# Kernel optimization log

Measured on AMD Instinct MI355X. Metric: run time of the kernel, lower is better.

Reference implementation:

```python
import jax, jax.numpy as jnp
import numpy as np

B, S, HID = 4, 1024, 2048
H, KV, D = 16, 4, 128  # query heads, kv heads, head_dim
ROPE_THETA = 1e6


def setup_inputs() -> dict:
    key = jax.random.key(0)
    ks = jax.random.split(key, 5)
    x = jax.random.normal(ks[0], (B, S, HID), dtype=jnp.float32)
    wq = jax.random.normal(ks[1], (HID, H * D), dtype=jnp.float32) / np.sqrt(HID)
    wk = jax.random.normal(ks[2], (HID, KV * D), dtype=jnp.float32) / np.sqrt(HID)
    wv = jax.random.normal(ks[3], (HID, KV * D), dtype=jnp.float32) / np.sqrt(HID)
    wo = jax.random.normal(ks[4], (H * D, HID), dtype=jnp.float32) / np.sqrt(H * D)
    # RoPE tables: freqs duplicated to head_dim (HF convention matching rotate_half)
    inv_freq = 1.0 / (ROPE_THETA ** (jnp.arange(0, D, 2, dtype=jnp.float32) / D))
    ang = jnp.arange(S, dtype=jnp.float32)[:, None] * inv_freq[None, :]  # [S, D/2]
    emb = jnp.concatenate([ang, ang], axis=-1)  # [S, D]
    return {"x": x, "cos": jnp.cos(emb), "sin": jnp.sin(emb),
            "wq": wq, "wk": wk, "wv": wv, "wo": wo}


def _rotate_half(t):
    half = t.shape[-1] // 2
    return jnp.concatenate([-t[..., half:], t[..., :half]], axis=-1)


def reference(x, cos, sin, wq, wk, wv, wo):
    b, s, _ = x.shape
    q = (x @ wq).reshape(b, s, H, D)
    k = (x @ wk).reshape(b, s, KV, D)
    v = (x @ wv).reshape(b, s, KV, D)
    # RoPE: cos/sin [S,D] broadcast over heads (unsqueeze_dim=1 -> [S,1,D])
    c = cos[:, None, :]
    sn = sin[:, None, :]
    q = q * c + _rotate_half(q) * sn
    k = k * c + _rotate_half(k) * sn
    # repeat_kv: each kv head repeated n_repeat times consecutively
    rep = H // KV
    k = jnp.repeat(k, rep, axis=2)  # [B,S,H,D]
    v = jnp.repeat(v, rep, axis=2)
    # [B,H,S,D]
    q = q.transpose(0, 2, 1, 3)
    k = k.transpose(0, 2, 1, 3)
    v = v.transpose(0, 2, 1, 3)
    scores = jnp.einsum("bhqd,bhkd->bhqk", q, k) / jnp.sqrt(jnp.float32(D))
    causal = jnp.tril(jnp.ones((s, s), dtype=bool))
    scores = jnp.where(causal, scores, -jnp.inf)
    probs = jax.nn.softmax(scores.astype(jnp.float32), axis=-1).astype(q.dtype)
    out = jnp.einsum("bhqk,bhkd->bhqd", probs, v)
    out = out.transpose(0, 2, 1, 3).reshape(b, s, H * D)
    return out @ wo
```

## Files before the change

kernel.cpp:

```cpp
#include <hip/hip_runtime.h>

typedef __attribute__((ext_vector_type(8))) __bf16 bf16x8;
typedef __attribute__((ext_vector_type(4))) __bf16 bf16x4;
typedef __attribute__((ext_vector_type(4))) float f32x4;

#define DEV static __device__ __forceinline__

DEV void gload_lds16(const void* g, void* l) {
  __builtin_amdgcn_global_load_lds((const __attribute__((address_space(1))) void*)g,
                                   (__attribute__((address_space(3))) void*)l, 16, 0, 0);
}

DEV void lgkm0_sb() {
  asm volatile("s_waitcnt lgkmcnt(0)" ::: "memory");
  __builtin_amdgcn_sched_barrier(0);
}

__global__ void cvt_kernel(const float* __restrict__ src, __bf16* __restrict__ dst, int n) {
  int i = (blockIdx.x * 256 + threadIdx.x) * 8;
  if (i >= n) return;
  float4 a = *(const float4*)(src + i);
  float4 b = *(const float4*)(src + i + 4);
  bf16x8 o;
  o[0] = (__bf16)a.x; o[1] = (__bf16)a.y; o[2] = (__bf16)a.z; o[3] = (__bf16)a.w;
  o[4] = (__bf16)b.x; o[5] = (__bf16)b.y; o[6] = (__bf16)b.z; o[7] = (__bf16)b.w;
  *(bf16x8*)(dst + i) = o;
}

__global__ void tcvt_kernel(const float* __restrict__ src, __bf16* __restrict__ dst, int K, int N) {
  __shared__ float tile[32][33];
  int k0 = blockIdx.y * 32, n0 = blockIdx.x * 32;
  int tx = threadIdx.x & 31, ty = threadIdx.x >> 5;
  #pragma unroll
  for (int i = 0; i < 32; i += 8)
    tile[ty + i][tx] = src[(size_t)(k0 + ty + i) * N + n0 + tx];
  __syncthreads();
  #pragma unroll
  for (int i = 0; i < 32; i += 8)
    dst[(size_t)(n0 + ty + i) * K + k0 + tx] = (__bf16)tile[tx][ty + i];
}

__global__ void vt_kernel(const __bf16* __restrict__ QKV, __bf16* __restrict__ VT) {
  __shared__ __bf16 t[32][33];
  int sx = blockIdx.x;
  int dx = blockIdx.y;
  int bk = blockIdx.z;
  int b = bk >> 2, kvh = bk & 3;
  int tx = threadIdx.x & 31, ty = threadIdx.x >> 5;
  #pragma unroll
  for (int i = 0; i < 32; i += 8)
    t[ty + i][tx] = QKV[(size_t)(b * 1024 + sx * 32 + ty + i) * 3072 + 2560 + kvh * 128 + dx * 32 + tx];
  __syncthreads();
  #pragma unroll
  for (int i = 0; i < 32; i += 8)
    VT[((size_t)bk * 128 + dx * 32 + ty + i) * 1024 + sx * 32 + tx] = t[tx][ty + i];
}

template <int BM, typename OutT>
__global__ __launch_bounds__(512, 2) void gemm8p(const __bf16* __restrict__ A,
                                                 const __bf16* __restrict__ Bt,
                                                 OutT* __restrict__ C,
                                                 int M, int N, int K) {
  constexpr int ABYTES = BM * 64 * 2;
  constexpr int BBYTES = 256 * 64 * 2;
  constexpr int MH = BM / 64;
  __shared__ alignas(1024) char smem[2 * (ABYTES + BBYTES)];

  const int tid = threadIdx.x;
  const int l = tid & 63, w = tid >> 6;
  const int wr = w >> 2, wc = w & 3;
  const int g = l >> 4, ln = l & 15;

  const int nbx = gridDim.x;
  const int nwg = nbx * gridDim.y;
  int lin = blockIdx.y * nbx + blockIdx.x;
  lin = (lin & 7) * (nwg >> 3) + (lin >> 3);
  const int brow = (lin / nbx) * BM, bcol = (lin % nbx) * 256;

  const __bf16* Ag = A + (size_t)brow * K;
  const __bf16* Bg = Bt + (size_t)bcol * K;
  const int NT = K / 64;

  auto Abuf = [&](int buf) -> char* { return smem + buf * ABYTES; };
  auto Bbuf = [&](int buf) -> char* { return smem + 2 * ABYTES + buf * BBYTES; };

  f32x4 acc[2 * MH][4] = {};

  auto chunk = [&](const __bf16* gb, char* lb, int ktc, int sub) {
    int r16 = l >> 2;
    int colb = ((l & 3) * 16) ^ (((l >> 5) & 1) << 5);
    int row = (sub >> 1) * 16 + r16;
    gload_lds16(gb + (size_t)row * K + ktc * 64 + (sub & 1) * 32 + (colb >> 1),
                lb + sub * 1024 + l * 16);
  };
  auto stA0 = [&](int ktc, int buf) {
    if constexpr (BM == 256) {
      #pragma unroll
      for (int i = 0; i < 2; ++i) { int idx = i * 8 + w; chunk(Ag, Abuf(buf), ktc, (idx >> 3) * 16 + (idx & 7)); }
    } else {
      chunk(Ag, Abuf(buf), ktc, (w >> 2) * 8 + (w & 3));
    }
  };
  auto stA1 = [&](int ktc, int buf) {
    if constexpr (BM == 256) {
      #pragma unroll
      for (int i = 0; i < 2; ++i) { int idx = i * 8 + w; chunk(Ag, Abuf(buf), ktc, 8 + (idx >> 3) * 16 + (idx & 7)); }
    } else {
      chunk(Ag, Abuf(buf), ktc, 4 + (w >> 2) * 8 + (w & 3));
    }
  };
  auto stB0 = [&](int ktc, int buf) {
    #pragma unroll
    for (int i = 0; i < 2; ++i) { int idx = i * 8 + w; chunk(Bg, Bbuf(buf), ktc, (idx >> 2) * 8 + (idx & 3)); }
  };
  auto stB1 = [&](int ktc, int buf) {
    #pragma unroll
    for (int i = 0; i < 2; ++i) { int idx = i * 8 + w; chunk(Bg, Bbuf(buf), ktc, 4 + (idx >> 2) * 8 + (idx & 3)); }
  };

  auto ldA = [&](int buf, int m, int kk) -> bf16x8 {
    int sub = (wr * (BM / 32) + m) * 2 + kk;
    return *(const bf16x8*)(Abuf(buf) + sub * 1024 + ln * 64 + ((g * 16) ^ (((ln >> 3) & 1) << 5)));
  };
  auto ldB = [&](int buf, int n, int kk) -> bf16x8 {
    int sub = (wc * 4 + n) * 2 + kk;
    return *(const bf16x8*)(Bbuf(buf) + sub * 1024 + ln * 64 + ((g * 16) ^ (((ln >> 3) & 1) << 5)));
  };

  auto vmw = [&](int which) {
    if constexpr (BM == 256) {
      if (which == 0) asm volatile("s_waitcnt vmcnt(10)" ::: "memory");
      else if (which == 1) asm volatile("s_waitcnt vmcnt(12)" ::: "memory");
      else asm volatile("s_waitcnt vmcnt(12)" ::: "memory");
    } else {
      if (which == 0) asm volatile("s_waitcnt vmcnt(7)" ::: "memory");
      else if (which == 1) asm volatile("s_waitcnt vmcnt(9)" ::: "memory");
      else asm volatile("s_waitcnt vmcnt(9)" ::: "memory");
    }
    __builtin_amdgcn_sched_barrier(0);
  };
  auto bar = [&]() {
    __builtin_amdgcn_sched_barrier(0);
    __builtin_amdgcn_s_barrier();
    __builtin_amdgcn_sched_barrier(0);
  };

  stA0(0, 0); stB0(0, 0); stB1(0, 0); stA1(0, 0);
  stA0(1, 1); stB0(1, 1); stB1(1, 1); stA1(1, 1);
  vmw(2);
  bar();

  bf16x8 af[MH][2], bf[4][2];

  for (int kt = 0; kt < NT; ++kt) {
    const int buf = kt & 1;
    const int ktc = (kt + 2) & 31;

    #pragma unroll
    for (int m = 0; m < MH; ++m) { af[m][0] = ldA(buf, m, 0); af[m][1] = ldA(buf, m, 1); }
    #pragma unroll
    for (int n = 0; n < 2; ++n) { bf[n][0] = ldB(buf, n, 0); bf[n][1] = ldB(buf, n, 1); }
    bar();
    lgkm0_sb();
    __builtin_amdgcn_s_setprio(1);
    #pragma unroll
    for (int m = 0; m < MH; ++m)
      #pragma unroll
      for (int n = 0; n < 2; ++n)
        #pragma unroll
        for (int kk = 0; kk < 2; ++kk)
          acc[m][n] = __builtin_amdgcn_mfma_f32_16x16x32_bf16(af[m][kk], bf[n][kk], acc[m][n], 0, 0, 0);
    __builtin_amdgcn_s_setprio(0);
    vmw(0);
    bar();

    #pragma unroll
    for (int n = 2; n < 4; ++n) { bf[n][0] = ldB(buf, n, 0); bf[n][1] = ldB(buf, n, 1); }
    stA0(ktc, buf); stB0(ktc, buf);
    bar();
    lgkm0_sb();
    __builtin_amdgcn_s_setprio(1);
    #pragma unroll
    for (int m = 0; m < MH; ++m)
      #pragma unroll
      for (int n = 2; n < 4; ++n)
        #pragma unroll
        for (int kk = 0; kk < 2; ++kk)
          acc[m][n] = __builtin_amdgcn_mfma_f32_16x16x32_bf16(af[m][kk], bf[n][kk], acc[m][n], 0, 0, 0);
    __builtin_amdgcn_s_setprio(0);
    vmw(1);
    bar();

    #pragma unroll
    for (int m = 0; m < MH; ++m) { af[m][0] = ldA(buf, MH + m, 0); af[m][1] = ldA(buf, MH + m, 1); }
    stB1(ktc, buf);
    bar();
    lgkm0_sb();
    __builtin_amdgcn_s_setprio(1);
    #pragma unroll
    for (int m = 0; m < MH; ++m)
      #pragma unroll
      for (int n = 0; n < 2; ++n)
        #pragma unroll
        for (int kk = 0; kk < 2; ++kk)
          acc[MH + m][n] = __builtin_amdgcn_mfma_f32_16x16x32_bf16(af[m][kk], bf[n][kk], acc[MH + m][n], 0, 0, 0);
    __builtin_amdgcn_s_setprio(0);
    bar();

    stA1(ktc, buf);
    bar();
    lgkm0_sb();
    __builtin_amdgcn_s_setprio(1);
    #pragma unroll
    for (int m = 0; m < MH; ++m)
      #pragma unroll
      for (int n = 2; n < 4; ++n)
        #pragma unroll
        for (int kk = 0; kk < 2; ++kk)
          acc[MH + m][n] = __builtin_amdgcn_mfma_f32_16x16x32_bf16(af[m][kk], bf[n][kk], acc[MH + m][n], 0, 0, 0);
    __builtin_amdgcn_s_setprio(0);
    vmw(2);
    bar();
  }

  #pragma unroll
  for (int mi = 0; mi < 2 * MH; ++mi)
    #pragma unroll
    for (int n = 0; n < 4; ++n)
      #pragma unroll
      for (int j = 0; j < 4; ++j) {
        size_t r = brow + wr * (BM / 2) + mi * 16 + g * 4 + j;
        size_t c = bcol + wc * 64 + n * 16 + ln;
        C[r * N + c] = (OutT)acc[mi][n][j];
      }
}

__global__ void rope_kernel(__bf16* __restrict__ QKV, const float* __restrict__ cosb,
                            const float* __restrict__ sinb) {
  int gid = blockIdx.x * 256 + threadIdx.x;
  int p = gid & 15;
  int ht = gid >> 4;
  int hc = ht % 20;
  int tok = ht / 20;
  int s = tok & 1023;
  int colb = hc < 16 ? hc * 128 : 2048 + (hc - 16) * 128;
  __bf16* base = QKV + (size_t)tok * 3072 + colb;
  int d0 = p * 4;
  const float* cr = cosb + s * 128;
  const float* sr = sinb + s * 128;
  float x0[4], x1[4];
  #pragma unroll
  for (int j = 0; j < 4; ++j) {
    x0[j] = (float)base[d0 + j];
    x1[j] = (float)base[d0 + 64 + j];
  }
  #pragma unroll
  for (int j = 0; j < 4; ++j) {
    float n0 = x0[j] * cr[d0 + j] - x1[j] * sr[d0 + j];
    float n1 = x1[j] * cr[d0 + 64 + j] + x0[j] * sr[d0 + 64 + j];
    base[d0 + j] = (__bf16)n0;
    base[d0 + 64 + j] = (__bf16)n1;
  }
}

__global__ __launch_bounds__(256, 2) void attn_kernel(const __bf16* __restrict__ QKV,
                                                      const __bf16* __restrict__ VT,
                                                      __bf16* __restrict__ AO) {
  __shared__ __bf16 Kl[2][64 * 128];
  __shared__ __bf16 Vt[128 * 64];
  __shared__ __bf16 Pl[4][16 * 72];

  const int tid = threadIdx.x, l = tid & 63, w = tid >> 6;
  const int h = blockIdx.y, b = blockIdx.z;
  const int kvh = h >> 2;
  const int g = l >> 4, ln = l & 15;
  const __bf16* VTg = VT + (size_t)(b * 4 + kvh) * 128 * 1024;
  const float scsc = 0.08838834764831845f;

  auto stageK = [&](int buf, int kt) {
    const __bf16* Kg = QKV + (size_t)(b * 1024 + kt * 64) * 3072 + 2048 + kvh * 128;
    #pragma unroll
    for (int i = 0; i < 4; ++i) {
      int r = i * 16 + (tid >> 4);
      int c = tid & 15;
      int csw = c ^ (r & 7);
      gload_lds16(Kg + (size_t)r * 3072 + csw * 8, (char*)&Kl[buf][0] + i * 4096 + tid * 16);
    }
  };
  auto stageV = [&](int kt) {
    #pragma unroll
    for (int i = 0; i < 4; ++i) {
      int ci = i * 256 + tid;
      int row = ci >> 3;
      int c = ci & 7;
      int csw = c ^ (row & 7);
      gload_lds16(VTg + (size_t)row * 1024 + kt * 64 + csw * 8, (char*)Vt + (size_t)ci * 16);
    }
  };

  #pragma unroll 1
  for (int pass = 0; pass < 2; ++pass) {
    const int qt = pass ? 15 - (int)blockIdx.x : (int)blockIdx.x;
    const size_t tokQ = (size_t)b * 1024 + qt * 64;

    bf16x8 qf[4];
    {
      const __bf16* qp = QKV + (tokQ + w * 16 + ln) * 3072 + h * 128;
      #pragma unroll
      for (int ks = 0; ks < 4; ++ks) qf[ks] = *(const bf16x8*)(qp + ks * 32 + g * 8);
    }

    float mrow = -1e30f, lrow = 0.f;
    f32x4 acco[8] = {};

    stageK(0, 0);
    int cur = 0;

    for (int kt = 0; kt <= qt; ++kt) {
      __syncthreads();

      stageV(kt);
      if (kt < qt) stageK(cur ^ 1, kt + 1);

      f32x4 accs[4] = {};
      __builtin_amdgcn_s_setprio(1);
      #pragma unroll
      for (int cb = 0; cb < 4; ++cb) {
        int row = cb * 16 + ln;
        #pragma unroll
        for (int ks = 0; ks < 4; ++ks) {
          bf16x8 kb = *(const bf16x8*)((const char*)&Kl[cur][0] + row * 256 +
                                       (((ks * 4 + g) ^ (row & 7)) * 16));
          accs[cb] = __builtin_amdgcn_mfma_f32_16x16x32_bf16(kb, qf[ks], accs[cb], 0, 0, 0);
        }
      }
      __builtin_amdgcn_s_setprio(0);

      const bool diag = (kt == qt);
      #pragma unroll
      for (int cb = 0; cb < 4; ++cb)
        #pragma unroll
        for (int j = 0; j < 4; ++j) {
          float s = accs[cb][j] * scsc;
          if (diag && (cb * 16 + g * 4 + j > w * 16 + ln)) s = -1e30f;
          accs[cb][j] = s;
        }

      float mt = accs[0][0];
      #pragma unroll
      for (int cb = 0; cb < 4; ++cb)
        #pragma unroll
        for (int j = 0; j < 4; ++j) mt = fmaxf(mt, accs[cb][j]);
      mt = fmaxf(mt, __shfl_xor(mt, 16, 64));
      mt = fmaxf(mt, __shfl_xor(mt, 32, 64));
      float mnew = fmaxf(mrow, mt);
      float corr = __expf(mrow - mnew);
      mrow = mnew;
      float rs = 0.f;
      #pragma unroll
      for (int cb = 0; cb < 4; ++cb)
        #pragma unroll
        for (int j = 0; j < 4; ++j) {
          float p = __expf(accs[cb][j] - mnew);
          accs[cb][j] = p;
          rs += p;
        }
      rs += __shfl_xor(rs, 16, 64);
      rs += __shfl_xor(rs, 32, 64);
      lrow = lrow * corr + rs;
      #pragma unroll
      for (int n = 0; n < 8; ++n)
        #pragma unroll
        for (int j = 0; j < 4; ++j) acco[n][j] *= corr;

      #pragma unroll
      for (int cb = 0; cb < 4; ++cb) {
        bf16x4 pw;
        #pragma unroll
        for (int j = 0; j < 4; ++j) pw[j] = (__bf16)accs[cb][j];
        *(bf16x4*)(&Pl[w][ln * 72 + cb * 16 + g * 4]) = pw;
      }

      __syncthreads();

      __builtin_amdgcn_s_setprio(1);
      #pragma unroll
      for (int sc = 0; sc < 2; ++sc) {
        bf16x8 pa = *(const bf16x8*)(&Pl[w][ln * 72 + sc * 32 + g * 8]);
        #pragma unroll
        for (int n = 0; n < 8; ++n) {
          int row = n * 16 + ln;
          bf16x8 vb = *(const bf16x8*)((const char*)Vt + row * 128 +
                                       (((sc * 4 + g) ^ (row & 7)) * 16));
          acco[n] = __builtin_amdgcn_mfma_f32_16x16x32_bf16(vb, pa, acco[n], 0, 0, 0);
        }
      }
      __builtin_amdgcn_s_setprio(0);
      cur ^= 1;
    }

    float rl = 1.f / lrow;
    size_t r = tokQ + w * 16 + ln;
    #pragma unroll
    for (int n = 0; n < 8; ++n) {
      bf16x4 ov;
      #pragma unroll
      for (int j = 0; j < 4; ++j) ov[j] = (__bf16)(acco[n][j] * rl);
      *(bf16x4*)(&AO[r * 2048 + h * 128 + n * 16 + g * 4]) = ov;
    }
  }
}

extern "C" void kernel_launch(void* const* d_in, const int* in_sizes, int n_in,
                              void* d_out, int out_size, void* d_ws, size_t ws_size,
                              hipStream_t stream) {
  const float* x    = (const float*)d_in[0];
  const float* cosb = (const float*)d_in[1];
  const float* sinb = (const float*)d_in[2];
  const float* wq   = (const float*)d_in[3];
  const float* wk   = (const float*)d_in[4];
  const float* wv   = (const float*)d_in[5];
  const float* wo   = (const float*)d_in[6];
  float* out = (float*)d_out;

  char* ws = (char*)d_ws;
  const size_t OFF_XB    = 0;
  const size_t OFF_WQKVT = OFF_XB + 16777216;
  const size_t OFF_WOT   = OFF_WQKVT + 12582912;
  const size_t OFF_QKV   = OFF_WOT + 8388608;
  const size_t OFF_AO    = OFF_QKV + 25165824;
  const size_t OFF_VT    = OFF_XB;

  __bf16* Xb    = (__bf16*)(ws + OFF_XB);
  __bf16* WqkvT = (__bf16*)(ws + OFF_WQKVT);
  __bf16* WoT   = (__bf16*)(ws + OFF_WOT);
  __bf16* QKVb  = (__bf16*)(ws + OFF_QKV);
  __bf16* AOb   = (__bf16*)(ws + OFF_AO);
  __bf16* VTb   = (__bf16*)(ws + OFF_VT);

  cvt_kernel<<<4096 * 2048 / 8 / 256, 256, 0, stream>>>(x, Xb, 4096 * 2048);
  tcvt_kernel<<<dim3(64, 64), 256, 0, stream>>>(wq, WqkvT, 2048, 2048);
  tcvt_kernel<<<dim3(16, 64), 256, 0, stream>>>(wk, WqkvT + (size_t)2048 * 2048, 2048, 512);
  tcvt_kernel<<<dim3(16, 64), 256, 0, stream>>>(wv, WqkvT + (size_t)2560 * 2048, 2048, 512);
  tcvt_kernel<<<dim3(64, 64), 256, 0, stream>>>(wo, WoT, 2048, 2048);
  gemm8p<256, __bf16><<<dim3(12, 16), 512, 0, stream>>>(Xb, WqkvT, QKVb, 4096, 3072, 2048);
  vt_kernel<<<dim3(32, 4, 16), 256, 0, stream>>>(QKVb, VTb);
  rope_kernel<<<4096 * 20 * 16 / 256, 256, 0, stream>>>(QKVb, cosb, sinb);
  attn_kernel<<<dim3(8, 16, 4), 256, 0, stream>>>(QKVb, VTb, AOb);
  gemm8p<128, float><<<dim3(8, 32), 512, 0, stream>>>(AOb, WoT, out, 4096, 2048, 2048);
}
```

Measured before the change: 175.3 us.

## Add dedicated 256x192-tile QKV GEMM so the grid fills all CUs

Adds a specialized QKV projection GEMM that uses 256x192 output tiles instead of 256x256, raising the grid from 192 to 256 workgroups so all 256 CUs on the MI355X get work. It reorganizes the staged global-to-LDS loads, the MFMA sub-phases and the vmcnt wait counts for the 3-wide N fragment per wave. The cost is some loss of data reuse per tile and hand-tuned wait counts, and the kernel hardcodes the K-tile wraparound ((kt+2)&31), so it assumes K=2048.

Result: no change. 172.3 us (-1.7%).

```diff
diff --git a/kernel.cpp b/kernel.cpp
--- a/kernel.cpp
+++ b/kernel.cpp
@@ -232,6 +232,166 @@
         size_t r = brow + wr * (BM / 2) + mi * 16 + g * 4 + j;
         size_t c = bcol + wc * 64 + n * 16 + ln;
         C[r * N + c] = (OutT)acc[mi][n][j];
+      }
+}
+
+__global__ __launch_bounds__(512, 2) void gemm8p_qkv(const __bf16* __restrict__ A,
+                                                     const __bf16* __restrict__ Bt,
+                                                     __bf16* __restrict__ C,
+                                                     int M, int N, int K) {
+  constexpr int ABYTES = 256 * 64 * 2;
+  constexpr int BBYTES = 192 * 64 * 2;
+  __shared__ alignas(1024) char smem[2 * (ABYTES + BBYTES)];
+
+  const int tid = threadIdx.x;
+  const int l = tid & 63, w = tid >> 6;
+  const int wr = w >> 2, wc = w & 3;
+  const int g = l >> 4, ln = l & 15;
+
+  const int nbx = gridDim.x;
+  const int nwg = nbx * gridDim.y;
+  int lin = blockIdx.y * nbx + blockIdx.x;
+  lin = (lin & 7) * (nwg >> 3) + (lin >> 3);
+  const int brow = (lin / nbx) * 256, bcol = (lin % nbx) * 192;
+
+  const __bf16* Ag = A + (size_t)brow * K;
+  const __bf16* Bg = Bt + (size_t)bcol * K;
+  const int NT = K / 64;
+
+  auto Abuf = [&](int buf) -> char* { return smem + buf * ABYTES; };
+  auto Bbuf = [&](int buf) -> char* { return smem + 2 * ABYTES + buf * BBYTES; };
+
+  f32x4 acc[8][3] = {};
+
+  auto chunk = [&](const __bf16* gb, char* lb, int ktc, int sub) {
+    int r16 = l >> 2;
+    int colb = ((l & 3) * 16) ^ (((l >> 5) & 1) << 5);
+    int row = (sub >> 1) * 16 + r16;
+    gload_lds16(gb + (size_t)row * K + ktc * 64 + (sub & 1) * 32 + (colb >> 1),
+                lb + sub * 1024 + l * 16);
+  };
+  auto stA0 = [&](int ktc, int buf) {
+    #pragma unroll
+    for (int i = 0; i < 2; ++i) { int idx = i * 8 + w; chunk(Ag, Abuf(buf), ktc, (idx >> 3) * 16 + (idx & 7)); }
+  };
+  auto stA1 = [&](int ktc, int buf) {
+    #pragma unroll
+    for (int i = 0; i < 2; ++i) { int idx = i * 8 + w; chunk(Ag, Abuf(buf), ktc, 8 + (idx >> 3) * 16 + (idx & 7)); }
+  };
+  auto stBg0 = [&](int ktc, int buf) {
+    #pragma unroll
+    for (int i = 0; i < 2; ++i) {
+      int t = i * 8 + w;
+      int sub = ((t >> 2) * 3 + ((t >> 1) & 1)) * 2 + (t & 1);
+      chunk(Bg, Bbuf(buf), ktc, sub);
+    }
+  };
+  auto stBg1 = [&](int ktc, int buf) {
+    int sub = ((w >> 1) * 3 + 2) * 2 + (w & 1);
+    chunk(Bg, Bbuf(buf), ktc, sub);
+  };
+
+  auto ldA = [&](int buf, int m, int kk) -> bf16x8 {
+    int sub = (wr * 8 + m) * 2 + kk;
+    return *(const bf16x8*)(Abuf(buf) + sub * 1024 + ln * 64 + ((g * 16) ^ (((ln >> 3) & 1) << 5)));
+  };
+  auto ldB = [&](int buf, int nf, int kk) -> bf16x8 {
+    int sub = (wc * 3 + nf) * 2 + kk;
+    return *(const bf16x8*)(Bbuf(buf) + sub * 1024 + ln * 64 + ((g * 16) ^ (((ln >> 3) & 1) << 5)));
+  };
+
+  auto bar = [&]() {
+    __builtin_amdgcn_sched_barrier(0);
+    __builtin_amdgcn_s_barrier();
+    __builtin_amdgcn_sched_barrier(0);
+  };
+
+  stA0(0, 0); stBg0(0, 0); stBg1(0, 0); stA1(0, 0);
+  stA0(1, 1); stBg0(1, 1); stBg1(1, 1); stA1(1, 1);
+  asm volatile("s_waitcnt vmcnt(10)" ::: "memory");
+  __builtin_amdgcn_sched_barrier(0);
+  bar();
+
+  bf16x8 af[4][2], bfv[3][2];
+
+  for (int kt = 0; kt < NT; ++kt) {
+    const int buf = kt & 1;
+    const int ktc = (kt + 2) & 31;
+
+    #pragma unroll
+    for (int m = 0; m < 4; ++m) { af[m][0] = ldA(buf, m, 0); af[m][1] = ldA(buf, m, 1); }
+    #pragma unroll
+    for (int nf = 0; nf < 2; ++nf) { bfv[nf][0] = ldB(buf, nf, 0); bfv[nf][1] = ldB(buf, nf, 1); }
+    bar();
+    lgkm0_sb();
+    __builtin_amdgcn_s_setprio(1);
+    #pragma unroll
+    for (int m = 0; m < 4; ++m)
+      #pragma unroll
+      for (int nf = 0; nf < 2; ++nf)
+        #pragma unroll
+        for (int kk = 0; kk < 2; ++kk)
+          acc[m][nf] = __builtin_amdgcn_mfma_f32_16x16x32_bf16(af[m][kk], bfv[nf][kk], acc[m][nf], 0, 0, 0);
+    __builtin_amdgcn_s_setprio(0);
+    asm volatile("s_waitcnt vmcnt(9)" ::: "memory");
+    __builtin_amdgcn_sched_barrier(0);
+    bar();
+
+    bfv[2][0] = ldB(buf, 2, 0); bfv[2][1] = ldB(buf, 2, 1);
+    stA0(ktc, buf); stBg0(ktc, buf);
+    bar();
+    lgkm0_sb();
+    __builtin_amdgcn_s_setprio(1);
+    #pragma unroll
+    for (int m = 0; m < 4; ++m)
+      #pragma unroll
+      for (int kk = 0; kk < 2; ++kk)
+        acc[m][2] = __builtin_amdgcn_mfma_f32_16x16x32_bf16(af[m][kk], bfv[2][kk], acc[m][2], 0, 0, 0);
+    __builtin_amdgcn_s_setprio(0);
+    asm volatile("s_waitcnt vmcnt(11)" ::: "memory");
+    __builtin_amdgcn_sched_barrier(0);
+    bar();
+
+    #pragma unroll
+    for (int m = 0; m < 4; ++m) { af[m][0] = ldA(buf, 4 + m, 0); af[m][1] = ldA(buf, 4 + m, 1); }
+    stBg1(ktc, buf);
+    bar();
+    lgkm0_sb();
+    __builtin_amdgcn_s_setprio(1);
+    #pragma unroll
+    for (int m = 0; m < 4; ++m)
+      #pragma unroll
+      for (int nf = 0; nf < 2; ++nf)
+        #pragma unroll
+        for (int kk = 0; kk < 2; ++kk)
+          acc[4 + m][nf] = __builtin_amdgcn_mfma_f32_16x16x32_bf16(af[m][kk], bfv[nf][kk], acc[4 + m][nf], 0, 0, 0);
+    __builtin_amdgcn_s_setprio(0);
+    bar();
+
+    stA1(ktc, buf);
+    bar();
+    lgkm0_sb();
+    __builtin_amdgcn_s_setprio(1);
+    #pragma unroll
+    for (int m = 0; m < 4; ++m)
+      #pragma unroll
+      for (int kk = 0; kk < 2; ++kk)
+        acc[4 + m][2] = __builtin_amdgcn_mfma_f32_16x16x32_bf16(af[m][kk], bfv[2][kk], acc[4 + m][2], 0, 0, 0);
+    __builtin_amdgcn_s_setprio(0);
+    asm volatile("s_waitcnt vmcnt(10)" ::: "memory");
+    __builtin_amdgcn_sched_barrier(0);
+    bar();
+  }
+
+  #pragma unroll
+  for (int mi = 0; mi < 8; ++mi)
+    #pragma unroll
+    for (int nf = 0; nf < 3; ++nf)
+      #pragma unroll
+      for (int j = 0; j < 4; ++j) {
+        size_t r = brow + wr * 128 + mi * 16 + g * 4 + j;
+        size_t c = bcol + wc * 48 + nf * 16 + ln;
+        C[r * N + c] = (__bf16)acc[mi][nf][j];
       }
 }
 
@@ -443,7 +603,7 @@
   tcvt_kernel<<<dim3(16, 64), 256, 0, stream>>>(wk, WqkvT + (size_t)2048 * 2048, 2048, 512);
   tcvt_kernel<<<dim3(16, 64), 256, 0, stream>>>(wv, WqkvT + (size_t)2560 * 2048, 2048, 512);
   tcvt_kernel<<<dim3(64, 64), 256, 0, stream>>>(wo, WoT, 2048, 2048);
-  gemm8p<256, __bf16><<<dim3(12, 16), 512, 0, stream>>>(Xb, WqkvT, QKVb, 4096, 3072, 2048);
+  gemm8p_qkv<<<dim3(16, 16), 512, 0, stream>>>(Xb, WqkvT, QKVb, 4096, 3072, 2048);
   vt_kernel<<<dim3(32, 4, 16), 256, 0, stream>>>(QKVb, VTb);
   rope_kernel<<<4096 * 20 * 16 / 256, 256, 0, stream>>>(QKVb, cosb, sinb);
   attn_kernel<<<dim3(8, 16, 4), 256, 0, stream>>>(QKVb, VTb, AOb);
```

## Retile GEMMs to 256-row tiles with narrower N and fuse Q RoPE into attention

Applied to the files above, without the earlier changes.

Replaces the GEMM kernel with a variant that uses 256-row A tiles and a 192- or 128-wide N tile, with a reworked four-phase K-split pipeline, so both projection GEMMs launch 256 workgroups instead of 192 or 256 with different shapes. This aims for better CU occupancy and wave balance on the GPU. It also moves the RoPE rotation of Q into the attention kernel's Q fragment load, so the standalone RoPE pass only handles K, which cuts global memory traffic. The risk is lower arithmetic intensity per tile and changed vmcnt accounting in the new pipeline.

Result: no change. 177.9 us (+1.5%).

```diff
diff --git a/kernel.cpp b/kernel.cpp
--- a/kernel.cpp
+++ b/kernel.cpp
@@ -56,14 +56,14 @@
     VT[((size_t)bk * 128 + dx * 32 + ty + i) * 1024 + sx * 32 + tx] = t[tx][ty + i];
 }
 
-template <int BM, typename OutT>
-__global__ __launch_bounds__(512, 2) void gemm8p(const __bf16* __restrict__ A,
+template <int NF, typename OutT>
+__global__ __launch_bounds__(512, 2) void gemm4s(const __bf16* __restrict__ A,
                                                  const __bf16* __restrict__ Bt,
                                                  OutT* __restrict__ C,
                                                  int M, int N, int K) {
-  constexpr int ABYTES = BM * 64 * 2;
-  constexpr int BBYTES = 256 * 64 * 2;
-  constexpr int MH = BM / 64;
+  constexpr int BN = NF * 64;
+  constexpr int ABYTES = 256 * 64 * 2;
+  constexpr int BBYTES = BN * 64 * 2;
   __shared__ alignas(1024) char smem[2 * (ABYTES + BBYTES)];
 
   const int tid = threadIdx.x;
@@ -75,7 +75,7 @@
   const int nwg = nbx * gridDim.y;
   int lin = blockIdx.y * nbx + blockIdx.x;
   lin = (lin & 7) * (nwg >> 3) + (lin >> 3);
-  const int brow = (lin / nbx) * BM, bcol = (lin % nbx) * 256;
+  const int brow = (lin / nbx) * 256, bcol = (lin % nbx) * BN;
 
   const __bf16* Ag = A + (size_t)brow * K;
   const __bf16* Bg = Bt + (size_t)bcol * K;
@@ -84,7 +84,7 @@
   auto Abuf = [&](int buf) -> char* { return smem + buf * ABYTES; };
   auto Bbuf = [&](int buf) -> char* { return smem + 2 * ABYTES + buf * BBYTES; };
 
-  f32x4 acc[2 * MH][4] = {};
+  f32x4 acc[8][NF] = {};
 
   auto chunk = [&](const __bf16* gb, char* lb, int ktc, int sub) {
     int r16 = l >> 2;
@@ -93,50 +93,35 @@
     gload_lds16(gb + (size_t)row * K + ktc * 64 + (sub & 1) * 32 + (colb >> 1),
                 lb + sub * 1024 + l * 16);
   };
-  auto stA0 = [&](int ktc, int buf) {
-    if constexpr (BM == 256) {
-      #pragma unroll
-      for (int i = 0; i < 2; ++i) { int idx = i * 8 + w; chunk(Ag, Abuf(buf), ktc, (idx >> 3) * 16 + (idx & 7)); }
+  auto stA = [&](int ktc, int buf, int kk) {
+    #pragma unroll
+    for (int i = 0; i < 2; ++i) { int t = i * 8 + w; chunk(Ag, Abuf(buf), ktc, t * 2 + kk); }
+  };
+  auto stB = [&](int ktc, int buf, int kk) {
+    if constexpr (NF == 3) {
+      #pragma unroll
+      for (int i = 0; i < 2; ++i) {
+        int t = i * 8 + w;
+        int s16 = t < 12 ? t : t - 4;
+        chunk(Bg, Bbuf(buf), ktc, s16 * 2 + kk);
+      }
     } else {
-      chunk(Ag, Abuf(buf), ktc, (w >> 2) * 8 + (w & 3));
-    }
-  };
-  auto stA1 = [&](int ktc, int buf) {
-    if constexpr (BM == 256) {
-      #pragma unroll
-      for (int i = 0; i < 2; ++i) { int idx = i * 8 + w; chunk(Ag, Abuf(buf), ktc, 8 + (idx >> 3) * 16 + (idx & 7)); }
-    } else {
-      chunk(Ag, Abuf(buf), ktc, 4 + (w >> 2) * 8 + (w & 3));
-    }
-  };
-  auto stB0 = [&](int ktc, int buf) {
-    #pragma unroll
-    for (int i = 0; i < 2; ++i) { int idx = i * 8 + w; chunk(Bg, Bbuf(buf), ktc, (idx >> 2) * 8 + (idx & 3)); }
-  };
-  auto stB1 = [&](int ktc, int buf) {
-    #pragma unroll
-    for (int i = 0; i < 2; ++i) { int idx = i * 8 + w; chunk(Bg, Bbuf(buf), ktc, 4 + (idx >> 2) * 8 + (idx & 3)); }
-  };
-
-  auto ldA = [&](int buf, int m, int kk) -> bf16x8 {
-    int sub = (wr * (BM / 32) + m) * 2 + kk;
+      chunk(Bg, Bbuf(buf), ktc, w * 2 + kk);
+    }
+  };
+
+  auto ldA = [&](int buf, int mi, int kk) -> bf16x8 {
+    int sub = (wr * 8 + mi) * 2 + kk;
     return *(const bf16x8*)(Abuf(buf) + sub * 1024 + ln * 64 + ((g * 16) ^ (((ln >> 3) & 1) << 5)));
   };
-  auto ldB = [&](int buf, int n, int kk) -> bf16x8 {
-    int sub = (wc * 4 + n) * 2 + kk;
+  auto ldB = [&](int buf, int nf, int kk) -> bf16x8 {
+    int sub = (wc * NF + nf) * 2 + kk;
     return *(const bf16x8*)(Bbuf(buf) + sub * 1024 + ln * 64 + ((g * 16) ^ (((ln >> 3) & 1) << 5)));
   };
 
-  auto vmw = [&](int which) {
-    if constexpr (BM == 256) {
-      if (which == 0) asm volatile("s_waitcnt vmcnt(10)" ::: "memory");
-      else if (which == 1) asm volatile("s_waitcnt vmcnt(12)" ::: "memory");
-      else asm volatile("s_waitcnt vmcnt(12)" ::: "memory");
-    } else {
-      if (which == 0) asm volatile("s_waitcnt vmcnt(7)" ::: "memory");
-      else if (which == 1) asm volatile("s_waitcnt vmcnt(9)" ::: "memory");
-      else asm volatile("s_waitcnt vmcnt(9)" ::: "memory");
-    }
+  auto vmN = [&]() {
+    if constexpr (NF == 3) asm volatile("s_waitcnt vmcnt(6)" ::: "memory");
+    else                   asm volatile("s_waitcnt vmcnt(4)" ::: "memory");
     __builtin_amdgcn_sched_barrier(0);
   };
   auto bar = [&]() {
@@ -145,106 +130,101 @@
     __builtin_amdgcn_sched_barrier(0);
   };
 
-  stA0(0, 0); stB0(0, 0); stB1(0, 0); stA1(0, 0);
-  stA0(1, 1); stB0(1, 1); stB1(1, 1); stA1(1, 1);
-  vmw(2);
+  stA(0, 0, 0); stB(0, 0, 0); stB(0, 0, 1); stA(0, 0, 1);
+  stA(1, 1, 0); stB(1, 1, 0); stB(1, 1, 1);
+  vmN();
   bar();
 
-  bf16x8 af[MH][2], bf[4][2];
+  bf16x8 af[4], bfv[NF];
 
   for (int kt = 0; kt < NT; ++kt) {
     const int buf = kt & 1;
-    const int ktc = (kt + 2) & 31;
-
-    #pragma unroll
-    for (int m = 0; m < MH; ++m) { af[m][0] = ldA(buf, m, 0); af[m][1] = ldA(buf, m, 1); }
-    #pragma unroll
-    for (int n = 0; n < 2; ++n) { bf[n][0] = ldB(buf, n, 0); bf[n][1] = ldB(buf, n, 1); }
+    const int kt1 = (kt + 1) & 31;
+    const int kt2 = (kt + 2) & 31;
+
+    #pragma unroll
+    for (int mi = 0; mi < 4; ++mi) af[mi] = ldA(buf, mi, 0);
+    #pragma unroll
+    for (int nf = 0; nf < NF; ++nf) bfv[nf] = ldB(buf, nf, 0);
+    stA(kt1, buf ^ 1, 1);
     bar();
     lgkm0_sb();
     __builtin_amdgcn_s_setprio(1);
     #pragma unroll
-    for (int m = 0; m < MH; ++m)
-      #pragma unroll
-      for (int n = 0; n < 2; ++n)
-        #pragma unroll
-        for (int kk = 0; kk < 2; ++kk)
-          acc[m][n] = __builtin_amdgcn_mfma_f32_16x16x32_bf16(af[m][kk], bf[n][kk], acc[m][n], 0, 0, 0);
+    for (int mi = 0; mi < 4; ++mi)
+      #pragma unroll
+      for (int nf = 0; nf < NF; ++nf)
+        acc[mi][nf] = __builtin_amdgcn_mfma_f32_16x16x32_bf16(af[mi], bfv[nf], acc[mi][nf], 0, 0, 0);
     __builtin_amdgcn_s_setprio(0);
-    vmw(0);
-    bar();
-
-    #pragma unroll
-    for (int n = 2; n < 4; ++n) { bf[n][0] = ldB(buf, n, 0); bf[n][1] = ldB(buf, n, 1); }
-    stA0(ktc, buf); stB0(ktc, buf);
+    bar();
+
+    #pragma unroll
+    for (int mi = 0; mi < 4; ++mi) af[mi] = ldA(buf, 4 + mi, 0);
+    stB(kt2, buf, 0);
     bar();
     lgkm0_sb();
     __builtin_amdgcn_s_setprio(1);
     #pragma unroll
-    for (int m = 0; m < MH; ++m)
-      #pragma unroll
-      for (int n = 2; n < 4; ++n)
-        #pragma unroll
-        for (int kk = 0; kk < 2; ++kk)
-          acc[m][n] = __builtin_amdgcn_mfma_f32_16x16x32_bf16(af[m][kk], bf[n][kk], acc[m][n], 0, 0, 0);
+    for (int mi = 0; mi < 4; ++mi)
+      #pragma unroll
+      for (int nf = 0; nf < NF; ++nf)
+        acc[4 + mi][nf] = __builtin_amdgcn_mfma_f32_16x16x32_bf16(af[mi], bfv[nf], acc[4 + mi][nf], 0, 0, 0);
     __builtin_amdgcn_s_setprio(0);
-    vmw(1);
-    bar();
-
-    #pragma unroll
-    for (int m = 0; m < MH; ++m) { af[m][0] = ldA(buf, MH + m, 0); af[m][1] = ldA(buf, MH + m, 1); }
-    stB1(ktc, buf);
+    bar();
+
+    #pragma unroll
+    for (int mi = 0; mi < 4; ++mi) af[mi] = ldA(buf, mi, 1);
+    #pragma unroll
+    for (int nf = 0; nf < NF; ++nf) bfv[nf] = ldB(buf, nf, 1);
+    stA(kt2, buf, 0);
     bar();
     lgkm0_sb();
     __builtin_amdgcn_s_setprio(1);
     #pragma unroll
-    for (int m = 0; m < MH; ++m)
-      #pragma unroll
-      for (int n = 0; n < 2; ++n)
-        #pragma unroll
-        for (int kk = 0; kk < 2; ++kk)
-          acc[MH + m][n] = __builtin_amdgcn_mfma_f32_16x16x32_bf16(af[m][kk], bf[n][kk], acc[MH + m][n], 0, 0, 0);
+    for (int mi = 0; mi < 4; ++mi)
+      #pragma unroll
+      for (int nf = 0; nf < NF; ++nf)
+        acc[mi][nf] = __builtin_amdgcn_mfma_f32_16x16x32_bf16(af[mi], bfv[nf], acc[mi][nf], 0, 0, 0);
     __builtin_amdgcn_s_setprio(0);
     bar();
 
-    stA1(ktc, buf);
+    #pragma unroll
+    for (int mi = 0; mi < 4; ++mi) af[mi] = ldA(buf, 4 + mi, 1);
+    stB(kt2, buf, 1);
     bar();
     lgkm0_sb();
     __builtin_amdgcn_s_setprio(1);
     #pragma unroll
-    for (int m = 0; m < MH; ++m)
-      #pragma unroll
-      for (int n = 2; n < 4; ++n)
-        #pragma unroll
-        for (int kk = 0; kk < 2; ++kk)
-          acc[MH + m][n] = __builtin_amdgcn_mfma_f32_16x16x32_bf16(af[m][kk], bf[n][kk], acc[MH + m][n], 0, 0, 0);
+    for (int mi = 0; mi < 4; ++mi)
+      #pragma unroll
+      for (int nf = 0; nf < NF; ++nf)
+        acc[4 + mi][nf] = __builtin_amdgcn_mfma_f32_16x16x32_bf16(af[mi], bfv[nf], acc[4 + mi][nf], 0, 0, 0);
     __builtin_amdgcn_s_setprio(0);
-    vmw(2);
+    vmN();
     bar();
   }
 
   #pragma unroll
-  for (int mi = 0; mi < 2 * MH; ++mi)
-    #pragma unroll
-    for (int n = 0; n < 4; ++n)
+  for (int mi = 0; mi < 8; ++mi)
+    #pragma unroll
+    for (int nf = 0; nf < NF; ++nf)
       #pragma unroll
       for (int j = 0; j < 4; ++j) {
-        size_t r = brow + wr * (BM / 2) + mi * 16 + g * 4 + j;
-        size_t c = bcol + wc * 64 + n * 16 + ln;
-        C[r * N + c] = (OutT)acc[mi][n][j];
+        size_t r = brow + wr * 128 + mi * 16 + g * 4 + j;
+        size_t c = bcol + wc * (NF * 16) + nf * 16 + ln;
+        C[r * N + c] = (OutT)acc[mi][nf][j];
       }
 }
 
-__global__ void rope_kernel(__bf16* __restrict__ QKV, const float* __restrict__ cosb,
-                            const float* __restrict__ sinb) {
+__global__ void ropek_kernel(__bf16* __restrict__ QKV, const float* __restrict__ cosb,
+                             const float* __restrict__ sinb) {
   int gid = blockIdx.x * 256 + threadIdx.x;
   int p = gid & 15;
   int ht = gid >> 4;
-  int hc = ht % 20;
-  int tok = ht / 20;
+  int hc = ht & 3;
+  int tok = ht >> 2;
   int s = tok & 1023;
-  int colb = hc < 16 ? hc * 128 : 2048 + (hc - 16) * 128;
-  __bf16* base = QKV + (size_t)tok * 3072 + colb;
+  __bf16* base = QKV + (size_t)tok * 3072 + 2048 + hc * 128;
   int d0 = p * 4;
   const float* cr = cosb + s * 128;
   const float* sr = sinb + s * 128;
@@ -265,6 +245,8 @@
 
 __global__ __launch_bounds__(256, 2) void attn_kernel(const __bf16* __restrict__ QKV,
                                                       const __bf16* __restrict__ VT,
+                                                      const float* __restrict__ cosb,
+                                                      const float* __restrict__ sinb,
                                                       __bf16* __restrict__ AO) {
   __shared__ __bf16 Kl[2][64 * 128];
   __shared__ __bf16 Vt[128 * 64];
@@ -302,12 +284,26 @@
   for (int pass = 0; pass < 2; ++pass) {
     const int qt = pass ? 15 - (int)blockIdx.x : (int)blockIdx.x;
     const size_t tokQ = (size_t)b * 1024 + qt * 64;
+    const int srow = qt * 64 + w * 16 + ln;
 
     bf16x8 qf[4];
     {
       const __bf16* qp = QKV + (tokQ + w * 16 + ln) * 3072 + h * 128;
-      #pragma unroll
-      for (int ks = 0; ks < 4; ++ks) qf[ks] = *(const bf16x8*)(qp + ks * 32 + g * 8);
+      bf16x8 qraw[4];
+      #pragma unroll
+      for (int ks = 0; ks < 4; ++ks) qraw[ks] = *(const bf16x8*)(qp + ks * 32 + g * 8);
+      const float* cr = cosb + (size_t)srow * 128;
+      const float* sr = sinb + (size_t)srow * 128;
+      #pragma unroll
+      for (int ks2 = 0; ks2 < 2; ++ks2)
+        #pragma unroll
+        for (int j = 0; j < 8; ++j) {
+          int d = ks2 * 32 + g * 8 + j;
+          float lo = (float)qraw[ks2][j], hi = (float)qraw[ks2 + 2][j];
+          float c0 = cr[d], s0 = sr[d];
+          qf[ks2][j]     = (__bf16)(lo * c0 - hi * s0);
+          qf[ks2 + 2][j] = (__bf16)(hi * c0 + lo * s0);
+        }
     }
 
     float mrow = -1e30f, lrow = 0.f;
@@ -443,9 +439,9 @@
   tcvt_kernel<<<dim3(16, 64), 256, 0, stream>>>(wk, WqkvT + (size_t)2048 * 2048, 2048, 512);
   tcvt_kernel<<<dim3(16, 64), 256, 0, stream>>>(wv, WqkvT + (size_t)2560 * 2048, 2048, 512);
   tcvt_kernel<<<dim3(64, 64), 256, 0, stream>>>(wo, WoT, 2048, 2048);
-  gemm8p<256, __bf16><<<dim3(12, 16), 512, 0, stream>>>(Xb, WqkvT, QKVb, 4096, 3072, 2048);
+  gemm4s<3, __bf16><<<dim3(16, 16), 512, 0, stream>>>(Xb, WqkvT, QKVb, 4096, 3072, 2048);
   vt_kernel<<<dim3(32, 4, 16), 256, 0, stream>>>(QKVb, VTb);
-  rope_kernel<<<4096 * 20 * 16 / 256, 256, 0, stream>>>(QKVb, cosb, sinb);
-  attn_kernel<<<dim3(8, 16, 4), 256, 0, stream>>>(QKVb, VTb, AOb);
-  gemm8p<128, float><<<dim3(8, 32), 512, 0, stream>>>(AOb, WoT, out, 4096, 2048, 2048);
-}
+  ropek_kernel<<<4096 * 4 * 16 / 256, 256, 0, stream>>>(QKVb, cosb, sinb);
+  attn_kernel<<<dim3(8, 16, 4), 256, 0, stream>>>(QKVb, VTb, cosb, sinb, AOb);
+  gemm4s<2, float><<<dim3(16, 16), 512, 0, stream>>>(AOb, WoT, out, 4096, 2048, 2048);
+}
```
